# Kernel tuning notes

Measured on AMD Instinct MI355X. Metric: run time of the kernel, lower is better.

## Reference

```python
import jax, jax.numpy as jnp
import numpy as np

H = W = 128      # image_shape
B = 64           # batch_size
O = 32           # orbit_size
RADIANS = True   # args.radians
RADIAN_INIT = 1.57
AFFINE_INIT = 0.1


def setup_inputs() -> dict:
    key = jax.random.key(0)
    k1, k2 = jax.random.split(key)
    X = jax.random.normal(k1, (B, H * W), dtype=jnp.float32)
    eps = jax.random.uniform(k2, (O, 7), dtype=jnp.float32)
    base = np.array([3.14, 1.0, 1.0, 1.0, 1.0, 1.0, 1.0], np.float32)
    ident = np.array([RADIAN_INIT, 1.0, 1.0, 0.0, 0.0, 0.0, 0.0], np.float32)
    tmin = ident - AFFINE_INIT * base
    tmax = np.array([-RADIAN_INIT, 1.0, 1.0, 0.0, 0.0, 0.0, 0.0], np.float32) + AFFINE_INIT * base
    return {
        "X": X,
        "eps": eps,
        "theta_min": jnp.asarray(tmin)[None, :],
        "theta_max": jnp.asarray(tmax)[None, :],
    }


def _affine_entries(thetas):
    # thetas: [O, 7] = [angle, sx, sy, shear_x, shear_y, tx, ty]
    # A = R(angle) @ [[sx, px], [py, sy]]  (rotation * scale/shear), t = [tx, ty]
    ang, sx, sy, px, py, tx, ty = (thetas[:, i] for i in range(7))
    if not RADIANS:
        ang = ang * (np.pi / 180.0)
    c, s = jnp.cos(ang), jnp.sin(ang)
    a00 = c * sx - s * py
    a01 = c * px - s * sy
    a10 = s * sx + c * py
    a11 = s * px + c * sy
    return a00, a01, a10, a11, tx, ty


def reference(X, eps, theta_min, theta_max):
    # sample orbit thetas: [O, 7]
    thetas = theta_min + (theta_max - theta_min) * eps
    a00, a01, a10, a11, tx, ty = _affine_entries(thetas)

    imgs = X.reshape(-1, H, W)  # [B, H, W]

    # normalized sampling grid in [-1, 1]
    xg = jnp.linspace(-1.0, 1.0, W, dtype=X.dtype)
    yg = jnp.linspace(-1.0, 1.0, H, dtype=X.dtype)
    Yg, Xg = jnp.meshgrid(yg, xg, indexing="ij")  # [H, W]

    # affine-transformed source coords per orbit sample: [O, H, W]
    xs = a00[:, None, None] * Xg + a01[:, None, None] * Yg + tx[:, None, None]
    ys = a10[:, None, None] * Xg + a11[:, None, None] * Yg + ty[:, None, None]

    # to pixel coords (align-corners convention)
    x = (xs + 1.0) * (W - 1) * 0.5
    y = (ys + 1.0) * (H - 1) * 0.5

    x0f = jnp.floor(x)
    y0f = jnp.floor(y)
    wx = x - x0f
    wy = y - y0f
    x0 = jnp.clip(x0f.astype(jnp.int32), 0, W - 1)
    x1 = jnp.clip(x0f.astype(jnp.int32) + 1, 0, W - 1)
    y0 = jnp.clip(y0f.astype(jnp.int32), 0, H - 1)
    y1 = jnp.clip(y0f.astype(jnp.int32) + 1, 0, H - 1)

    # gather 4 corners: fancy index over all images at once -> [B, O, H, W]
    Ia = imgs[:, y0, x0]
    Ib = imgs[:, y1, x0]
    Ic = imgs[:, y0, x1]
    Id = imgs[:, y1, x1]

    wa = (1.0 - wx) * (1.0 - wy)
    wb = (1.0 - wx) * wy
    wc = wx * (1.0 - wy)
    wd = wx * wy

    out = Ia * wa + Ib * wb + Ic * wc + Id * wd  # [B, O, H, W]
    out = jnp.transpose(out, (1, 0, 2, 3))       # [O, B, H, W]: per-theta batches
    return out.reshape(B * O, H, W, 1)
```

## Files before the change

### kernel.cpp

```cpp
#include <hip/hip_runtime.h>

#define HH 128
#define WW 128
#define BB 64
#define OO 32

__launch_bounds__(1024, 8)
__global__ void sample_kernel(const float* __restrict__ X,
                              const float* __restrict__ eps,
                              const float* __restrict__ tmin,
                              const float* __restrict__ tmax,
                              float* __restrict__ out) {
    __shared__ float img[HH * WW];
    __shared__ float scoef[4][6];

    const int bid = blockIdx.x;
    const int og  = bid & 7;
    const int b   = bid >> 3;
    const int tid = threadIdx.x;

    if (tid < 4) {
        const int o = og * 4 + tid;
        float th[7];
#pragma unroll
        for (int i = 0; i < 7; ++i) {
            const float mn = tmin[i], mx = tmax[i];
            th[i] = mn + (mx - mn) * eps[o * 7 + i];
        }
        const float ang = th[0], sx = th[1], sy = th[2], px = th[3],
                    py = th[4], tx = th[5], ty = th[6];
        const float c = cosf(ang), s = sinf(ang);
        const float half = 0.5f * (WW - 1);
        scoef[tid][0] = (c * sx - s * py) * half;
        scoef[tid][1] = (c * px - s * sy) * half;
        scoef[tid][2] = (tx + 1.0f) * half;
        scoef[tid][3] = (s * sx + c * py) * half;
        scoef[tid][4] = (s * px + c * sy) * half;
        scoef[tid][5] = (ty + 1.0f) * half;
    }

    {
        const float4* __restrict__ src = (const float4*)(X + b * (HH * WW));
        float4* dst = (float4*)img;
#pragma unroll
        for (int i = 0; i < 4; ++i)
            dst[tid + i * 1024] = src[tid + i * 1024];
    }
    __syncthreads();

    const int w  = tid & (WW - 1);
    const int h0 = tid >> 7;
    const float step  = 2.0f / 127.0f;
    const float hstep = 8.0f * step;
    const float Xg  = -1.0f + w * step;
    const float Yg0 = -1.0f + h0 * step;
    const float hi  = 126.999992f;

#pragma unroll
    for (int j = 0; j < 4; ++j) {
        const int o = og * 4 + j;
        const float cx0 = scoef[j][0];
        const float cx1 = scoef[j][1];
        const float cxt = scoef[j][2];
        const float cy0 = scoef[j][3];
        const float cy1 = scoef[j][4];
        const float cyt = scoef[j][5];

        float x = fmaf(cx1, Yg0, fmaf(cx0, Xg, cxt));
        float y = fmaf(cy1, Yg0, fmaf(cy0, Xg, cyt));
        const float dx = cx1 * hstep;
        const float dy = cy1 * hstep;

        float* __restrict__ outp =
            out + ((size_t)(o * BB + b) * (HH * WW)) + h0 * WW + w;

#pragma unroll
        for (int i = 0; i < 16; ++i) {
            const float xc = __builtin_amdgcn_fmed3f(x, 0.0f, hi);
            const float yc = __builtin_amdgcn_fmed3f(y, 0.0f, hi);
            const float x0f = floorf(xc);
            const float y0f = floorf(yc);
            const float wx = xc - x0f;
            const float wy = yc - y0f;
            const int idx = (int)fmaf(y0f, 128.0f, x0f);

            const float Ia = img[idx];
            const float Ic = img[idx + 1];
            const float Ib = img[idx + WW];
            const float Id = img[idx + WW + 1];

            const float top = fmaf(wx, Ic - Ia, Ia);
            const float bot = fmaf(wx, Id - Ib, Ib);
            *outp = fmaf(wy, bot - top, top);

            outp += 8 * WW;
            x += dx;
            y += dy;
        }
    }
}

extern "C" void kernel_launch(void* const* d_in, const int* in_sizes, int n_in,
                              void* d_out, int out_size, void* d_ws, size_t ws_size,
                              hipStream_t stream) {
    const float* X    = (const float*)d_in[0];
    const float* eps  = (const float*)d_in[1];
    const float* tmin = (const float*)d_in[2];
    const float* tmax = (const float*)d_in[3];
    float* out = (float*)d_out;

    const int nblocks = BB * 8;
    sample_kernel<<<nblocks, 1024, 0, stream>>>(X, eps, tmin, tmax, out);
}
```

Measured before the change: 153.8 us.

## Compute four adjacent pixels per thread with float4 stores and packed math

Each thread now handles four horizontally adjacent output pixels and writes them with one float4 store instead of four scalar stores. The thread-to-pixel mapping changes from 128 columns by 8 rows to 32 quads by 32 rows. The x/y coordinate and lerp arithmetic is rewritten with 2-wide float vectors to encourage packed FP32 instructions. The aim is fewer store instructions and less ALU issue on a store-bound kernel. In exchange, LDS gather accesses within a wave become more strided, which may add bank conflicts.

After: 157.6 us. 2.5% more time.

```diff
diff --git a/kernel.cpp b/kernel.cpp
--- a/kernel.cpp
+++ b/kernel.cpp
@@ -4,6 +4,8 @@
 #define WW 128
 #define BB 64
 #define OO 32
+
+typedef float v2f __attribute__((ext_vector_type(2)));
 
 __launch_bounds__(1024, 8)
 __global__ void sample_kernel(const float* __restrict__ X,
@@ -48,11 +50,10 @@
     }
     __syncthreads();
 
-    const int w  = tid & (WW - 1);
-    const int h0 = tid >> 7;
-    const float step  = 2.0f / 127.0f;
-    const float hstep = 8.0f * step;
-    const float Xg  = -1.0f + w * step;
+    const int w4 = (tid & 31) << 2;
+    const int h0 = tid >> 5;
+    const float step = 2.0f / 127.0f;
+    const float Xg0 = -1.0f + w4 * step;
     const float Yg0 = -1.0f + h0 * step;
     const float hi  = 126.999992f;
 
@@ -66,36 +67,46 @@
         const float cy1 = scoef[j][4];
         const float cyt = scoef[j][5];
 
-        float x = fmaf(cx1, Yg0, fmaf(cx0, Xg, cxt));
-        float y = fmaf(cy1, Yg0, fmaf(cy0, Xg, cyt));
-        const float dx = cx1 * hstep;
-        const float dy = cy1 * hstep;
+        v2f xy_row;
+        xy_row.x = fmaf(cx1, Yg0, fmaf(cx0, Xg0, cxt));
+        xy_row.y = fmaf(cy1, Yg0, fmaf(cy0, Xg0, cyt));
+        v2f dxy_w = {cx0 * step, cy0 * step};
+        v2f dxy_h = {cx1 * (32.0f * step), cy1 * (32.0f * step)};
 
-        float* __restrict__ outp =
-            out + ((size_t)(o * BB + b) * (HH * WW)) + h0 * WW + w;
+        float4* __restrict__ outp = (float4*)(
+            out + ((size_t)(o * BB + b) * (HH * WW)) + h0 * WW + w4);
 
 #pragma unroll
-        for (int i = 0; i < 16; ++i) {
-            const float xc = __builtin_amdgcn_fmed3f(x, 0.0f, hi);
-            const float yc = __builtin_amdgcn_fmed3f(y, 0.0f, hi);
-            const float x0f = floorf(xc);
-            const float y0f = floorf(yc);
-            const float wx = xc - x0f;
-            const float wy = yc - y0f;
-            const int idx = (int)fmaf(y0f, 128.0f, x0f);
+        for (int i = 0; i < 4; ++i) {
+            v2f xy = xy_row;
+            float4 r;
+            float* rp = &r.x;
+#pragma unroll
+            for (int p = 0; p < 4; ++p) {
+                v2f xyc;
+                xyc.x = __builtin_amdgcn_fmed3f(xy.x, 0.0f, hi);
+                xyc.y = __builtin_amdgcn_fmed3f(xy.y, 0.0f, hi);
+                const v2f fl  = __builtin_elementwise_floor(xyc);
+                const v2f wxy = xyc - fl;
+                const int idx = (int)fmaf(fl.y, 128.0f, fl.x);
 
-            const float Ia = img[idx];
-            const float Ic = img[idx + 1];
-            const float Ib = img[idx + WW];
-            const float Id = img[idx + WW + 1];
+                const float Ia = img[idx];
+                const float Ic = img[idx + 1];
+                const float Ib = img[idx + WW];
+                const float Id = img[idx + WW + 1];
 
-            const float top = fmaf(wx, Ic - Ia, Ia);
-            const float bot = fmaf(wx, Id - Ib, Ib);
-            *outp = fmaf(wy, bot - top, top);
+                const v2f AB = {Ia, Ib};
+                const v2f CD = {Ic, Id};
+                const v2f d  = CD - AB;
+                const v2f wxx = {wxy.x, wxy.x};
+                const v2f r2 = __builtin_elementwise_fma(wxx, d, AB);
+                rp[p] = fmaf(wxy.y, r2.y - r2.x, r2.x);
 
-            outp += 8 * WW;
-            x += dx;
-            y += dy;
+                xy += dxy_w;
+            }
+            *outp = r;
+            outp += 32 * WW / 4;
+            xy_row += dxy_h;
         }
     }
 }
```
